# Optimization experiments

Measured on AMD Instinct MI355X. Metric: run time of the kernel, lower is better.

The kernel has to match this reference:

```python
import jax, jax.numpy as jnp
import numpy as np

# config.lattice_hash constants
BOX = 32.0          # box_length
D = 64              # num_divisions (hash grid per dim)
NPV = 2             # num_points_1d_per_bin_voxel
L = D * NPV         # dense lattice side = 128
T = 8               # number_of_atom_types
GW = 0.3            # gauss_width
BUFFER_FACTOR = 2
N = 1_048_576
NUM_BINS = D ** 3
CAP = int(np.ceil(BUFFER_FACTOR * N / NUM_BINS))  # 8 slots per bin


def setup_inputs() -> dict:
    key = jax.random.key(0)
    k1, k2 = jax.random.split(key)
    points = jax.random.uniform(k1, (N, 3), jnp.float32) * BOX  # coords in [0, BOX)
    mask = jnp.ones((N,), bool)
    atom_types = jax.random.randint(k2, (N,), 0, T, jnp.int32)
    return {"points": points, "mask": mask, "atom_types": atom_types}


def _spatial_hash(points, mask):
    """Bucket points into D^3 spatial bins with a fixed per-bin buffer (capacity CAP)."""
    cell = jnp.clip(jnp.floor(points / BOX * D).astype(jnp.int32), 0, D - 1)  # [N,3]
    bin_id = (cell[:, 0] * D + cell[:, 1]) * D + cell[:, 2]                    # [N]
    bin_id = jnp.where(mask, bin_id, NUM_BINS)  # masked points -> overflow bucket
    order = jnp.argsort(bin_id)
    sb = bin_id[order]          # sorted bin ids
    sp = points[order]          # points in bin order
    first = jnp.searchsorted(sb, sb, side="left")   # first index of each bin run
    slot = jnp.arange(N, dtype=jnp.int32) - first.astype(jnp.int32)  # rank within bin
    valid = (sb < NUM_BINS) & (slot < CAP)
    b = jnp.where(valid, sb, 0)
    s = jnp.where(valid, slot, 0)
    vf = valid.astype(points.dtype)
    buffer_ = jnp.zeros((NUM_BINS, CAP, 3), points.dtype).at[b, s].add(sp * vf[:, None])
    buffer_mask = (jnp.zeros((NUM_BINS, CAP), points.dtype).at[b, s].add(vf) > 0)
    counts = jax.ops.segment_sum(mask.astype(jnp.int32), bin_id, num_segments=NUM_BINS + 1)[:NUM_BINS]
    return buffer_, buffer_mask, counts


def _splat_to_lattice(points, mask, atom_types):
    """Gaussian density splat of points onto dense [L,L,L,T] lattice (27-cell window)."""
    cell = jnp.floor(points / BOX * L).astype(jnp.int32)  # [N,3]
    r = jnp.arange(-1, 2)
    offs = jnp.stack(jnp.meshgrid(r, r, r, indexing="ij"), -1).reshape(-1, 3)  # [27,3]
    c = cell[:, None, :] + offs[None].astype(jnp.int32)   # [N,27,3]
    inb = jnp.all((c >= 0) & (c < L), axis=-1)            # [N,27]
    cc = jnp.clip(c, 0, L - 1)
    centers = (cc.astype(points.dtype) + 0.5) * (BOX / L)  # voxel centers
    d2 = jnp.sum((points[:, None, :] - centers) ** 2, axis=-1)  # [N,27]
    w = jnp.exp(-d2 / (2.0 * GW * GW)) * inb * mask[:, None]
    flat = ((cc[..., 0] * L + cc[..., 1]) * L + cc[..., 2]) * T + atom_types[:, None]
    lat = jnp.zeros((L * L * L * T,), points.dtype).at[flat.reshape(-1)].add(w.reshape(-1))
    return lat.reshape(L, L, L, T)


def reference(points, mask, atom_types):
    buffer_, buffer_mask, _counts = _spatial_hash(points, mask)
    dense_lattice = _splat_to_lattice(points, mask, atom_types)
    return (dense_lattice, buffer_, buffer_mask)
```

## Files before the change

### kernel.cpp

```cpp
#include <hip/hip_runtime.h>
#include <hip/hip_bf16.h>
#include <climits>

#define N_PTS     1048576
#define DDIV      64
#define ZCELLS    128
#define NUM_BINS  (DDIV*DDIV*DDIV)
#define NCB       (DDIV*DDIV*ZCELLS)
#define CAP       8
#define TTYPES    8
#define LSIDE     128
#define TCAP      32
#define LAT_ELEMS (LSIDE*LSIDE*LSIDE*TTYPES)
#define BUF_ELEMS (NUM_BINS*CAP*3)
#define NBLK2     (NCB/256)
#define NPAIRS    (LSIDE*LSIDE*(LSIDE/2))
#define EMIT_BLKS (NUM_BINS/256)

#define INV2GW2  5.5555555555555554f
#define K2EXP2   8.0149707f
#define VOX      0.25f
#define HASH_SCALE 2.0f
#define LAT_SCALE  4.0f

typedef float f32x2 __attribute__((ext_vector_type(2)));

__device__ __forceinline__ int cell_of(float x, float y, float z) {
    int cx = min(max((int)floorf(x * HASH_SCALE), 0), DDIV-1);
    int cy = min(max((int)floorf(y * HASH_SCALE), 0), DDIV-1);
    int cz = min(max((int)floorf(z * LAT_SCALE), 0), ZCELLS-1);
    return (cx * DDIV + cy) * ZCELLS + cz;
}

__device__ __forceinline__ int bin_of(float x, float y, float z) {
    int cx = min(max((int)floorf(x * HASH_SCALE), 0), DDIV-1);
    int cy = min(max((int)floorf(y * HASH_SCALE), 0), DDIV-1);
    int cz = min(max((int)floorf(z * HASH_SCALE), 0), DDIV-1);
    return (cx * DDIV + cy) * DDIV + cz;
}


__global__ void count_kernel(const float* __restrict__ pts,
                             int* __restrict__ counts) {
    int i = blockIdx.x * blockDim.x + threadIdx.x;
    const float4* p4 = (const float4*)(pts + (size_t)i * 12);
    float4 a = p4[0], b = p4[1], c = p4[2];
    atomicAdd(&counts[cell_of(a.x, a.y, a.z)], 1);
    atomicAdd(&counts[cell_of(a.w, b.x, b.y)], 1);
    atomicAdd(&counts[cell_of(b.z, b.w, c.x)], 1);
    atomicAdd(&counts[cell_of(c.y, c.z, c.w)], 1);
}

__global__ void scan_block_kernel(const int* __restrict__ counts,
                                  int* __restrict__ start,
                                  int* __restrict__ bsums) {
    __shared__ int s[256];
    int tid = threadIdx.x;
    int gid = blockIdx.x * 256 + tid;
    int v = counts[gid];
    s[tid] = v; __syncthreads();
    for (int off = 1; off < 256; off <<= 1) {
        int t = (tid >= off) ? s[tid - off] : 0;
        __syncthreads();
        s[tid] += t;
        __syncthreads();
    }
    start[gid] = s[tid] - v;
    if (tid == 255) bsums[blockIdx.x] = s[255];
}

__global__ void finalize_kernel(int* __restrict__ start,
                                const int* __restrict__ bsums) {
    __shared__ int s[256];
    int tid = threadIdx.x;
    int b = blockIdx.x;
    int acc = 0;
    for (int i = tid; i < b; i += 256) acc += bsums[i];
    s[tid] = acc; __syncthreads();
    for (int off = 128; off > 0; off >>= 1) {
        if (tid < off) s[tid] += s[tid + off];
        __syncthreads();
    }
    int base = s[0];
    int gid = b * 256 + tid;
    start[gid] += base;
    if (gid == NCB - 1) start[NCB] = N_PTS;
}

__global__ void scatter_kernel(const float* __restrict__ pts,
                               const int* __restrict__ types,
                               const int* __restrict__ start,
                               int* __restrict__ counts,
                               float4* __restrict__ ps) {
    int i = blockIdx.x * blockDim.x + threadIdx.x;
    const float4* p4 = (const float4*)(pts + (size_t)i * 12);
    float4 a = p4[0], b = p4[1], c = p4[2];
    const int4 t4 = *(const int4*)(types + (size_t)i * 4);
    int i0 = i * 4;
    float px[4] = {a.x, a.w, b.z, c.y};
    float py[4] = {a.y, b.x, b.w, c.z};
    float pz[4] = {a.z, b.y, c.x, c.w};
    int   tt[4] = {t4.x, t4.y, t4.z, t4.w};
    #pragma unroll
    for (int k = 0; k < 4; ++k) {
        int bb = cell_of(px[k], py[k], pz[k]);
        int pos = start[bb] + atomicSub(&counts[bb], 1) - 1;
        ps[pos] = make_float4(px[k], py[k], pz[k],
                              __int_as_float(((i0 + k) << 3) | tt[k]));
    }
}

__global__ __launch_bounds__(256) void gather_emit_kernel(
        const float4* __restrict__ ps,
        const int* __restrict__ start,
        float* __restrict__ lat,
        float* __restrict__ buf,
        float* __restrict__ bmask) {
    int ltid = threadIdx.x;
    int bid  = blockIdx.x;
    int wid = ltid >> 6, lane = ltid & 63;

    if (bid < EMIT_BLKS) {
        int b = bid * 256 + wid * 64 + lane;
        int bz = b & 63, byy = (b >> 6) & 63, bxx = b >> 12;
        int cbase = (bxx * DDIV + byy) * ZCELLS + (bz << 1);
        int s0 = start[cbase], e0 = start[cbase + 2];
        int cnt = e0 - s0;
        if (cnt <= 8) {
            float4 pv[8]; int key[8], rk[8];
            #pragma unroll
            for (int k = 0; k < 8; ++k) {
                if (k < cnt) { pv[k] = ps[s0 + k]; key[k] = __float_as_int(pv[k].w); }
                else { pv[k] = make_float4(0.f,0.f,0.f,0.f); key[k] = INT_MAX; }
            }
            #pragma unroll
            for (int k = 0; k < 8; ++k) {
                int r = 0;
                #pragma unroll
                for (int j = 0; j < 8; ++j) r += (key[j] < key[k]);
                rk[k] = (k < cnt) ? r : 99;
            }
            float sx[8], sy[8], sz[8];
            #pragma unroll
            for (int s = 0; s < 8; ++s) {
                float vx = 0.f, vy = 0.f, vz = 0.f;
                #pragma unroll
                for (int k = 0; k < 8; ++k) {
                    bool pick = (rk[k] == s);
                    vx = pick ? pv[k].x : vx;
                    vy = pick ? pv[k].y : vy;
                    vz = pick ? pv[k].z : vz;
                }
                sx[s] = vx; sy[s] = vy; sz[s] = vz;
            }
            float4* ob = (float4*)(buf + (size_t)b * 24);
            ob[0] = make_float4(sx[0], sy[0], sz[0], sx[1]);
            ob[1] = make_float4(sy[1], sz[1], sx[2], sy[2]);
            ob[2] = make_float4(sz[2], sx[3], sy[3], sz[3]);
            ob[3] = make_float4(sx[4], sy[4], sz[4], sx[5]);
            ob[4] = make_float4(sy[5], sz[5], sx[6], sy[6]);
            ob[5] = make_float4(sz[6], sx[7], sy[7], sz[7]);
            float4* om = (float4*)(bmask + (size_t)b * 8);
            om[0] = make_float4(cnt>0?1.f:0.f, cnt>1?1.f:0.f, cnt>2?1.f:0.f, cnt>3?1.f:0.f);
            om[1] = make_float4(cnt>4?1.f:0.f, cnt>5?1.f:0.f, cnt>6?1.f:0.f, cnt>7?1.f:0.f);
        } else {
            int prev = INT_MIN;
            for (int s = 0; s < CAP; ++s) {
                int m = INT_MAX, mj = s0;
                for (int j = s0; j < e0; ++j) {
                    int u = __float_as_int(ps[j].w);
                    if (u > prev && u < m) { m = u; mj = j; }
                }
                prev = m;
                float4 p = ps[mj];
                int base = (b * CAP + s) * 3;
                buf[base+0] = p.x; buf[base+1] = p.y; buf[base+2] = p.z;
                bmask[b * CAP + s] = 1.f;
            }
        }
    }

    int tid = bid * 256 + ltid;
    int zp = tid & 63;
    int y  = (tid >> 6) & 127;
    int x  = tid >> 13;
    int z0 = zp * 2;

    float cxv = ((float)x  + 0.5f) * VOX;
    float cyv = ((float)y  + 0.5f) * VOX;
    float czv = ((float)z0 + 0.5f) * VOX;

    f32x2 acc[TTYPES];
    #pragma unroll
    for (int t = 0; t < TTYPES; ++t) acc[t] = (f32x2){0.f, 0.f};

    int bxs[2] = { (x-1) >> 1, (x+1) >> 1 };
    int bys[2] = { (y-1) >> 1, (y+1) >> 1 };
    int zlo = max(z0 - 1, 0);
    int zhi = min(z0 + 2, ZCELLS - 1);

    #pragma unroll
    for (int xi = 0; xi < 2; ++xi) {
        int bx = bxs[xi];
        if ((unsigned)bx >= (unsigned)DDIV) continue;
        #pragma unroll
        for (int yi = 0; yi < 2; ++yi) {
            int by = bys[yi];
            if ((unsigned)by >= (unsigned)DDIV) continue;
            int cb = (bx * DDIV + by) * ZCELLS;
            int lo = start[cb + zlo];
            int hi = start[cb + zhi + 1];
            for (int j = lo; j < hi; ++j) {
                float4 p = ps[j];
                int pcx = (int)(p.x * LAT_SCALE);
                int dxc = pcx - x;
                if (dxc < -1 || dxc > 1) continue;
                int pcy = (int)(p.y * LAT_SCALE);
                int dyc = pcy - y;
                if (dyc < -1 || dyc > 1) continue;
                float dx = p.x - cxv, dy = p.y - cyv;
                float dxy = fmaf(dx, dx, dy * dy);
                int pcz = (int)(p.z * LAT_SCALE);
                int dzc = pcz - z0;
                float dz0 = p.z - czv;
                float dz1 = dz0 - VOX;
                float w0 = (dzc <= 1) ? exp2f(-fmaf(dz0, dz0, dxy) * K2EXP2) : 0.f;
                float w1 = (dzc >= 0) ? exp2f(-fmaf(dz1, dz1, dxy) * K2EXP2) : 0.f;
                f32x2 w01 = (f32x2){w0, w1};
                int at = __float_as_int(p.w) & 7;
                #pragma unroll
                for (int t = 0; t < TTYPES; ++t) {
                    float sel = (at == t) ? 1.f : 0.f;
                    acc[t] += (f32x2){sel, sel} * w01;
                }
            }
        }
    }

    float4* o = (float4*)(lat + ((size_t)((x * LSIDE) + y) * LSIDE + z0) * TTYPES);
    o[0] = make_float4(acc[0].x, acc[1].x, acc[2].x, acc[3].x);
    o[1] = make_float4(acc[4].x, acc[5].x, acc[6].x, acc[7].x);
    o[2] = make_float4(acc[0].y, acc[1].y, acc[2].y, acc[3].y);
    o[3] = make_float4(acc[4].y, acc[5].y, acc[6].y, acc[7].y);
}


__global__ void hash_count_kernel(const float* __restrict__ pts,
                                  int* __restrict__ counts,
                                  int* __restrict__ temp) {
    int i = blockIdx.x * blockDim.x + threadIdx.x;
    if (i >= N_PTS) return;
    int bin = bin_of(pts[3*i], pts[3*i+1], pts[3*i+2]);
    int t = atomicAdd(&counts[bin], 1);
    if (t < TCAP) temp[bin * TCAP + t] = i;
}

__global__ void bin_emit_kernel_pts(const float* __restrict__ pts,
                                    const int* __restrict__ counts,
                                    const int* __restrict__ temp,
                                    float* __restrict__ buf,
                                    float* __restrict__ bmask) {
    int b = blockIdx.x * blockDim.x + threadIdx.x;
    if (b >= NUM_BINS) return;
    int cnt = counts[b];
    if (cnt > TCAP) cnt = TCAP;
    const int* t = temp + b * TCAP;
    int nOut = cnt < CAP ? cnt : CAP;
    int prev = -1;
    for (int s = 0; s < CAP; ++s) {
        float x = 0.f, y = 0.f, z = 0.f, mv = 0.f;
        if (s < nOut) {
            int m = INT_MAX;
            for (int j = 0; j < cnt; ++j) {
                int v = t[j];
                if (v > prev && v < m) m = v;
            }
            prev = m;
            x = pts[3*m+0]; y = pts[3*m+1]; z = pts[3*m+2];
            mv = 1.f;
        }
        int base = (b * CAP + s) * 3;
        buf[base+0] = x; buf[base+1] = y; buf[base+2] = z;
        bmask[b * CAP + s] = mv;
    }
}

__global__ void splat_kernel(const float* __restrict__ pts,
                             const int* __restrict__ types,
                             float* __restrict__ lat) {
    int i = blockIdx.x * blockDim.x + threadIdx.x;
    if (i >= N_PTS) return;
    float px = pts[3*i+0], py = pts[3*i+1], pz = pts[3*i+2];
    int cx = (int)floorf(px * LAT_SCALE);
    int cy = (int)floorf(py * LAT_SCALE);
    int cz = (int)floorf(pz * LAT_SCALE);
    int at = types[i];
    float wx[3], wy[3], wz[3];
    #pragma unroll
    for (int d = 0; d < 3; ++d) {
        int c = cx + d - 1;
        float ctr = ((float)c + 0.5f) * VOX;
        float dd = px - ctr;
        wx[d] = (c >= 0 && c < LSIDE) ? __expf(-dd*dd*INV2GW2) : 0.f;
        c = cy + d - 1; ctr = ((float)c + 0.5f) * VOX; dd = py - ctr;
        wy[d] = (c >= 0 && c < LSIDE) ? __expf(-dd*dd*INV2GW2) : 0.f;
        c = cz + d - 1; ctr = ((float)c + 0.5f) * VOX; dd = pz - ctr;
        wz[d] = (c >= 0 && c < LSIDE) ? __expf(-dd*dd*INV2GW2) : 0.f;
    }
    #pragma unroll
    for (int a = 0; a < 3; ++a) {
        if (wx[a] == 0.f) continue;
        int ix = cx + a - 1;
        #pragma unroll
        for (int b = 0; b < 3; ++b) {
            if (wy[b] == 0.f) continue;
            int iy = cy + b - 1;
            float wxy = wx[a] * wy[b];
            #pragma unroll
            for (int cdx = 0; cdx < 3; ++cdx) {
                if (wz[cdx] == 0.f) continue;
                int iz = cz + cdx - 1;
                float w = wxy * wz[cdx];
                int flat = ((ix * LSIDE + iy) * LSIDE + iz) * TTYPES + at;
                atomicAdd(&lat[flat], w);
            }
        }
    }
}


extern "C" void kernel_launch(void* const* d_in, const int* in_sizes, int n_in,
                              void* d_out, int out_size, void* d_ws, size_t ws_size,
                              hipStream_t stream) {
    const float* pts   = (const float*)d_in[0];
    const int*   types = (const int*)d_in[2];

    float* lat   = (float*)d_out;
    float* buf   = lat + LAT_ELEMS;
    float* bmask = buf + BUF_ELEMS;

    const size_t counts_off = 0;
    const size_t start_off  = counts_off + (size_t)NCB * 4;
    const size_t bsums_off  = start_off  + (size_t)(NCB + 1) * 4;
    size_t ps_off           = bsums_off  + (size_t)NBLK2 * 4;
    ps_off = (ps_off + 15) & ~(size_t)15;
    const size_t need = ps_off + (size_t)N_PTS * sizeof(float4);

    if (ws_size >= need) {
        int*    counts = (int*)((char*)d_ws + counts_off);
        int*    start  = (int*)((char*)d_ws + start_off);
        int*    bsums  = (int*)((char*)d_ws + bsums_off);
        float4* ps     = (float4*)((char*)d_ws + ps_off);

        hipMemsetAsync(counts, 0, (size_t)NCB * 4, stream);

        count_kernel<<<N_PTS / 4 / 256, 256, 0, stream>>>(pts, counts);
        scan_block_kernel<<<NBLK2, 256, 0, stream>>>(counts, start, bsums);
        finalize_kernel<<<NBLK2, 256, 0, stream>>>(start, bsums);
        scatter_kernel<<<N_PTS / 4 / 256, 256, 0, stream>>>(pts, types, start, counts, ps);
        gather_emit_kernel<<<NPAIRS / 256, 256, 0, stream>>>(ps, start, lat, buf, bmask);
    } else {
        int* counts = (int*)d_out;
        int* temp   = counts + NUM_BINS;
        hipMemsetAsync(counts, 0, (size_t)NUM_BINS * 4, stream);
        hash_count_kernel<<<N_PTS / 256, 256, 0, stream>>>(pts, counts, temp);
        bin_emit_kernel_pts<<<NUM_BINS / 256, 256, 0, stream>>>(
            pts, counts, temp, buf, bmask);
        hipMemsetAsync(lat, 0, (size_t)LAT_ELEMS * sizeof(float), stream);
        splat_kernel<<<N_PTS / 256, 256, 0, stream>>>(pts, types, lat);
    }
}
```

Before: 225.4 us.

## Fuse CSR build stages into one cooperative kernel with grid syncs

Replaces the memset, count, block-scan, finalize and scatter launches with a single cooperative kernel of 1024 blocks that runs a grid-stride loop for each stage and separates the stages with grid.sync(). The goal is to remove the launch gaps and per-kernel tail effects between five small dependent launches. In exchange it depends on cooperative launch support, so it falls back to the old sequence if the launch fails. Grid-wide barriers also have their own cost, and the serial bsums scan in block 0 idles the rest of the grid.

```diff
diff --git a/kernel.cpp b/kernel.cpp
--- a/kernel.cpp
+++ b/kernel.cpp
@@ -1,6 +1,9 @@
 #include <hip/hip_runtime.h>
 #include <hip/hip_bf16.h>
+#include <hip/hip_cooperative_groups.h>
 #include <climits>
+
+namespace cg = cooperative_groups;
 
 #define N_PTS     1048576
 #define DDIV      64
@@ -16,6 +19,7 @@
 #define NBLK2     (NCB/256)
 #define NPAIRS    (LSIDE*LSIDE*(LSIDE/2))
 #define EMIT_BLKS (NUM_BINS/256)
+#define COOP_BLKS 1024
 
 #define INV2GW2  5.5555555555555554f
 #define K2EXP2   8.0149707f
@@ -37,6 +41,89 @@
     int cy = min(max((int)floorf(y * HASH_SCALE), 0), DDIV-1);
     int cz = min(max((int)floorf(z * HASH_SCALE), 0), DDIV-1);
     return (cx * DDIV + cy) * DDIV + cz;
+}
+
+__global__ __launch_bounds__(256) void build_csr_coop(
+        const float* __restrict__ pts,
+        const int* __restrict__ types,
+        int* __restrict__ counts,
+        int* __restrict__ start,
+        int* __restrict__ bsums,
+        float4* __restrict__ ps) {
+    cg::grid_group grid = cg::this_grid();
+    __shared__ int s[256];
+    int tid = threadIdx.x;
+    int gtid = blockIdx.x * 256 + tid;
+    const int gsize = COOP_BLKS * 256;
+
+    for (int i = gtid; i < NCB; i += gsize) counts[i] = 0;
+    grid.sync();
+
+    for (int g = gtid; g < N_PTS / 4; g += gsize) {
+        const float4* p4 = (const float4*)(pts + (size_t)g * 12);
+        float4 a = p4[0], b = p4[1], c = p4[2];
+        atomicAdd(&counts[cell_of(a.x, a.y, a.z)], 1);
+        atomicAdd(&counts[cell_of(a.w, b.x, b.y)], 1);
+        atomicAdd(&counts[cell_of(b.z, b.w, c.x)], 1);
+        atomicAdd(&counts[cell_of(c.y, c.z, c.w)], 1);
+    }
+    grid.sync();
+
+    for (int chunk = blockIdx.x; chunk < NBLK2; chunk += COOP_BLKS) {
+        int gid = chunk * 256 + tid;
+        int v = counts[gid];
+        s[tid] = v; __syncthreads();
+        for (int off = 1; off < 256; off <<= 1) {
+            int t = (tid >= off) ? s[tid - off] : 0;
+            __syncthreads();
+            s[tid] += t;
+            __syncthreads();
+        }
+        start[gid] = s[tid] - v;
+        if (tid == 255) bsums[chunk] = s[255];
+        __syncthreads();
+    }
+    grid.sync();
+
+    if (blockIdx.x == 0) {
+        int base8 = tid * 8;
+        int v[8], sum = 0;
+        #pragma unroll
+        for (int k = 0; k < 8; ++k) { v[k] = bsums[base8 + k]; sum += v[k]; }
+        s[tid] = sum; __syncthreads();
+        for (int off = 1; off < 256; off <<= 1) {
+            int t = (tid >= off) ? s[tid - off] : 0;
+            __syncthreads();
+            s[tid] += t;
+            __syncthreads();
+        }
+        int run = s[tid] - sum;
+        #pragma unroll
+        for (int k = 0; k < 8; ++k) { int vv = v[k]; bsums[base8 + k] = run; run += vv; }
+    }
+    grid.sync();
+
+    for (int i = gtid; i < NCB; i += gsize) start[i] += bsums[i >> 8];
+    if (gtid == 0) start[NCB] = N_PTS;
+    grid.sync();
+
+    for (int g = gtid; g < N_PTS / 4; g += gsize) {
+        const float4* p4 = (const float4*)(pts + (size_t)g * 12);
+        float4 a = p4[0], b = p4[1], c = p4[2];
+        const int4 t4 = *(const int4*)(types + (size_t)g * 4);
+        int i0 = g * 4;
+        float px[4] = {a.x, a.w, b.z, c.y};
+        float py[4] = {a.y, b.x, b.w, c.z};
+        float pz[4] = {a.z, b.y, c.x, c.w};
+        int   tt[4] = {t4.x, t4.y, t4.z, t4.w};
+        #pragma unroll
+        for (int k = 0; k < 4; ++k) {
+            int bb = cell_of(px[k], py[k], pz[k]);
+            int pos = start[bb] + atomicSub(&counts[bb], 1) - 1;
+            ps[pos] = make_float4(px[k], py[k], pz[k],
+                                  __int_as_float(((i0 + k) << 3) | tt[k]));
+        }
+    }
 }
 
 
@@ -109,6 +196,7 @@
                               __int_as_float(((i0 + k) << 3) | tt[k]));
     }
 }
+
 
 __global__ __launch_bounds__(256) void gather_emit_kernel(
         const float4* __restrict__ ps,
@@ -352,12 +440,19 @@
         int*    bsums  = (int*)((char*)d_ws + bsums_off);
         float4* ps     = (float4*)((char*)d_ws + ps_off);
 
-        hipMemsetAsync(counts, 0, (size_t)NCB * 4, stream);
-
-        count_kernel<<<N_PTS / 4 / 256, 256, 0, stream>>>(pts, counts);
-        scan_block_kernel<<<NBLK2, 256, 0, stream>>>(counts, start, bsums);
-        finalize_kernel<<<NBLK2, 256, 0, stream>>>(start, bsums);
-        scatter_kernel<<<N_PTS / 4 / 256, 256, 0, stream>>>(pts, types, start, counts, ps);
+        void* args[] = { (void*)&pts, (void*)&types, (void*)&counts,
+                         (void*)&start, (void*)&bsums, (void*)&ps };
+        hipError_t cerr = hipLaunchCooperativeKernel(
+            (const void*)build_csr_coop, dim3(COOP_BLKS), dim3(256),
+            args, 0, stream);
+        if (cerr != hipSuccess) {
+            hipMemsetAsync(counts, 0, (size_t)NCB * 4, stream);
+            count_kernel<<<N_PTS / 4 / 256, 256, 0, stream>>>(pts, counts);
+            scan_block_kernel<<<NBLK2, 256, 0, stream>>>(counts, start, bsums);
+            finalize_kernel<<<NBLK2, 256, 0, stream>>>(start, bsums);
+            scatter_kernel<<<N_PTS / 4 / 256, 256, 0, stream>>>(
+                pts, types, start, counts, ps);
+        }
         gather_emit_kernel<<<NPAIRS / 256, 256, 0, stream>>>(ps, start, lat, buf, bmask);
     } else {
         int* counts = (int*)d_out;
```

Measured after the change: 698.7 us. 210% more time.

## Fuse scan and finalize via atomic cursor with unordered cell segments

Applied to the files above, without the earlier changes.

Replaces the two-pass prefix scan (block scan plus a finalize kernel that re-sums prior block totals) with a single kernel. Each block claims a base offset through an atomicAdd on a global cursor, so cell segments are no longer globally ordered. A separate ends array therefore stores each cell's segment end. Gather code now reads ends instead of start[next], which is correct only while segments that are read together stay contiguous within a 256-cell block. This removes a kernel launch and the finalize kernel's repeated reduction over block sums, at the cost of an extra array write and read.

```diff
diff --git a/kernel.cpp b/kernel.cpp
--- a/kernel.cpp
+++ b/kernel.cpp
@@ -51,10 +51,12 @@
     atomicAdd(&counts[cell_of(c.y, c.z, c.w)], 1);
 }
 
-__global__ void scan_block_kernel(const int* __restrict__ counts,
+__global__ void scan_fused_kernel(const int* __restrict__ counts,
                                   int* __restrict__ start,
-                                  int* __restrict__ bsums) {
+                                  int* __restrict__ ends,
+                                  int* __restrict__ cursor) {
     __shared__ int s[256];
+    __shared__ int basz;
     int tid = threadIdx.x;
     int gid = blockIdx.x * 256 + tid;
     int v = counts[gid];
@@ -65,26 +67,11 @@
         s[tid] += t;
         __syncthreads();
     }
-    start[gid] = s[tid] - v;
-    if (tid == 255) bsums[blockIdx.x] = s[255];
-}
-
-__global__ void finalize_kernel(int* __restrict__ start,
-                                const int* __restrict__ bsums) {
-    __shared__ int s[256];
-    int tid = threadIdx.x;
-    int b = blockIdx.x;
-    int acc = 0;
-    for (int i = tid; i < b; i += 256) acc += bsums[i];
-    s[tid] = acc; __syncthreads();
-    for (int off = 128; off > 0; off >>= 1) {
-        if (tid < off) s[tid] += s[tid + off];
-        __syncthreads();
-    }
-    int base = s[0];
-    int gid = b * 256 + tid;
-    start[gid] += base;
-    if (gid == NCB - 1) start[NCB] = N_PTS;
+    if (tid == 255) basz = atomicAdd(cursor, s[255]);
+    __syncthreads();
+    int base = basz;
+    start[gid] = base + s[tid] - v;
+    ends[gid]  = base + s[tid];
 }
 
 __global__ void scatter_kernel(const float* __restrict__ pts,
@@ -113,6 +100,7 @@
 __global__ __launch_bounds__(256) void gather_emit_kernel(
         const float4* __restrict__ ps,
         const int* __restrict__ start,
+        const int* __restrict__ ends,
         float* __restrict__ lat,
         float* __restrict__ buf,
         float* __restrict__ bmask) {
@@ -124,7 +112,7 @@
         int b = bid * 256 + wid * 64 + lane;
         int bz = b & 63, byy = (b >> 6) & 63, bxx = b >> 12;
         int cbase = (bxx * DDIV + byy) * ZCELLS + (bz << 1);
-        int s0 = start[cbase], e0 = start[cbase + 2];
+        int s0 = start[cbase], e0 = ends[cbase + 1];
         int cnt = e0 - s0;
         if (cnt <= 8) {
             float4 pv[8]; int key[8], rk[8];
@@ -209,7 +197,7 @@
             if ((unsigned)by >= (unsigned)DDIV) continue;
             int cb = (bx * DDIV + by) * ZCELLS;
             int lo = start[cb + zlo];
-            int hi = start[cb + zhi + 1];
+            int hi = ends[cb + zhi];
             for (int j = lo; j < hi; ++j) {
                 float4 p = ps[j];
                 int pcx = (int)(p.x * LAT_SCALE);
@@ -340,25 +328,27 @@
     float* bmask = buf + BUF_ELEMS;
 
     const size_t counts_off = 0;
-    const size_t start_off  = counts_off + (size_t)NCB * 4;
-    const size_t bsums_off  = start_off  + (size_t)(NCB + 1) * 4;
-    size_t ps_off           = bsums_off  + (size_t)NBLK2 * 4;
+    const size_t cursor_off = counts_off + (size_t)NCB * 4;
+    const size_t start_off  = cursor_off + 64;
+    const size_t ends_off   = start_off + (size_t)NCB * 4;
+    size_t ps_off           = ends_off + (size_t)NCB * 4;
     ps_off = (ps_off + 15) & ~(size_t)15;
     const size_t need = ps_off + (size_t)N_PTS * sizeof(float4);
 
     if (ws_size >= need) {
         int*    counts = (int*)((char*)d_ws + counts_off);
+        int*    cursor = (int*)((char*)d_ws + cursor_off);
         int*    start  = (int*)((char*)d_ws + start_off);
-        int*    bsums  = (int*)((char*)d_ws + bsums_off);
+        int*    ends   = (int*)((char*)d_ws + ends_off);
         float4* ps     = (float4*)((char*)d_ws + ps_off);
 
-        hipMemsetAsync(counts, 0, (size_t)NCB * 4, stream);
+        hipMemsetAsync(counts, 0, (size_t)NCB * 4 + 64, stream);
 
         count_kernel<<<N_PTS / 4 / 256, 256, 0, stream>>>(pts, counts);
-        scan_block_kernel<<<NBLK2, 256, 0, stream>>>(counts, start, bsums);
-        finalize_kernel<<<NBLK2, 256, 0, stream>>>(start, bsums);
+        scan_fused_kernel<<<NBLK2, 256, 0, stream>>>(counts, start, ends, cursor);
         scatter_kernel<<<N_PTS / 4 / 256, 256, 0, stream>>>(pts, types, start, counts, ps);
-        gather_emit_kernel<<<NPAIRS / 256, 256, 0, stream>>>(ps, start, lat, buf, bmask);
+        gather_emit_kernel<<<NPAIRS / 256, 256, 0, stream>>>(
+            ps, start, ends, lat, buf, bmask);
     } else {
         int* counts = (int*)d_out;
         int* temp   = counts + NUM_BINS;
```

After: 246.0 us. 9.1% more time.
